# Optimization experiments

Measured on AMD Instinct MI355X. Metric: run time of the kernel, lower is better.

Reference implementation:

```python
import jax, jax.numpy as jnp
import numpy as np

N_NODES = 65536
N_EDGES = 1048576
D_FEAT = 64
K_HOPS = 10
ALPHA = 0.1


def setup_inputs() -> dict:
    key = jax.random.key(0)
    k1, k2 = jax.random.split(key, 2)
    x = jax.random.normal(k1, (N_NODES, D_FEAT), dtype=jnp.float32)
    edge_index = jax.random.randint(k2, (2, N_EDGES), 0, N_NODES, dtype=jnp.int32)
    # PPR init of the learnable polynomial coefficients (length K+1)
    temp = ALPHA * (1.0 - ALPHA) ** np.arange(K_HOPS + 1)
    temp[-1] = (1.0 - ALPHA) ** K_HOPS
    temp = jnp.asarray(temp, dtype=jnp.float32)
    return {"x": x, "temp": temp, "edge_index": edge_index}


def reference(x, temp, edge_index):
    # GCN-normalized adjacency with self-loops (gcn_norm, homophily=True path):
    #   A_hat = D^{-1/2} (A + I) D^{-1/2}
    N = x.shape[0]
    K = temp.shape[0] - 1
    loops = jnp.arange(N, dtype=edge_index.dtype)
    src = jnp.concatenate([edge_index[0], loops])  # message sources (x_j)
    dst = jnp.concatenate([edge_index[1], loops])  # aggregation targets
    ones = jnp.ones(src.shape[0], dtype=x.dtype)
    deg = jax.ops.segment_sum(ones, dst, num_segments=N)  # self-loops => deg > 0
    dinv = jax.lax.rsqrt(deg)
    norm = dinv[src] * dinv[dst]  # [E+N]

    # hidden = temp[K-1]*x; then K-1 propagation hops accumulating temp[k]*A_hat^m x
    hidden = temp[K - 1] * x
    h = x
    for k in range(K - 2, -1, -1):
        # sparse propagate: scatter-add of norm-weighted gathered source features
        h = jax.ops.segment_sum(norm[:, None] * h[src], dst, num_segments=N)
        hidden = hidden + temp[k] * h
    return hidden
```

## Files before the change

### kernel.cpp

```cpp
#include <hip/hip_runtime.h>
#include <hip/hip_fp16.h>

#define N_NODES 65536
#define N_EDGES 1048576
#define BUCKET  64

typedef float vfloat4 __attribute__((ext_vector_type(4)));
typedef unsigned long long ull;


__global__ void count_deg(const int* __restrict__ dst, int* __restrict__ counts,
                          int* __restrict__ rank) {
    int e = blockIdx.x * blockDim.x + threadIdx.x;
    if (e < N_EDGES) rank[e] = atomicAdd(&counts[dst[e]], 1);
}

__global__ void compute_dinv(const int* __restrict__ counts, float* __restrict__ dinv) {
    int v = blockIdx.x * blockDim.x + threadIdx.x;
    if (v < N_NODES) dinv[v] = rsqrtf((float)(counts[v] + 1));
}

__global__ void scatter_src(const int* __restrict__ src, const int* __restrict__ dst,
                            const int* __restrict__ rank,
                            unsigned short* __restrict__ csr) {
    int e = blockIdx.x * blockDim.x + threadIdx.x;
    if (e >= N_EDGES) return;
    int r = rank[e];
    if (r < BUCKET) csr[dst[e] * BUCKET + r] = (unsigned short)src[e];
}

__global__ void cvt_x(const float* __restrict__ x, const float* __restrict__ dinv,
                      __half* __restrict__ t0, __half* __restrict__ xh) {
    int i = blockIdx.x * blockDim.x + threadIdx.x;
    int v = i >> 4;
    float dv = dinv[v];
    vfloat4 val = __builtin_nontemporal_load((const vfloat4*)x + i);
    __half2 xl = __floats2half2_rn(val.x, val.y);
    __half2 xh2 = __floats2half2_rn(val.z, val.w);
    ull ox = ((ull)(*(const unsigned*)&xh2) << 32) | (*(const unsigned*)&xl);
    __half2 tl = __floats2half2_rn(dv * val.x, dv * val.y);
    __half2 th = __floats2half2_rn(dv * val.z, dv * val.w);
    ull ot = ((ull)(*(const unsigned*)&th) << 32) | (*(const unsigned*)&tl);
    __builtin_nontemporal_store(ox, (ull*)xh + i);
    ((ull*)t0)[i] = ot;
}

__global__ void __launch_bounds__(256) hop_kernel(
        const __half* __restrict__ tab, const __half* __restrict__ xh,
        __half* __restrict__ tab_out, float* __restrict__ out_f32,
        const float* __restrict__ temp, const int* __restrict__ counts,
        const unsigned short* __restrict__ csr, const float* __restrict__ dinv,
        int k) {
    int gtid = blockIdx.x * blockDim.x + threadIdx.x;
    int wave = __builtin_amdgcn_readfirstlane(gtid >> 6);
    int lane = gtid & 63;
    int q = lane >> 4;
    int f = lane & 15;

    int v0 = wave * 4;
    float tk = temp[k];
    float sc = (k == 1) ? temp[0] : 1.0f;

    int4 cv = *(const int4*)(counts + v0);
    int cnt[4];
    cnt[0] = min(cv.x, BUCKET); cnt[1] = min(cv.y, BUCKET);
    cnt[2] = min(cv.z, BUCKET); cnt[3] = min(cv.w, BUCKET);
    float4 dvv = *(const float4*)(dinv + v0);
    float dv[4] = {dvv.x, dvv.y, dvv.z, dvv.w};

    int maxc = max(max(cnt[0], cnt[1]), max(cnt[2], cnt[3]));
    int iters = (maxc + 31) >> 5;

    const ull* t2 = (const ull*)tab;
    float a0[4] = {0.f, 0.f, 0.f, 0.f};
    float a1[4] = {0.f, 0.f, 0.f, 0.f};
    float a2[4] = {0.f, 0.f, 0.f, 0.f};
    float a3[4] = {0.f, 0.f, 0.f, 0.f};

    for (int r = 0; r < iters; ++r) {
        int e0 = r * 32;
        #pragma unroll
        for (int j = 0; j < 4; ++j) {
            const int4* bp = (const int4*)(csr + (v0 + j) * BUCKET + e0);
            int4 sg0 = bp[0];
            int4 sg1 = bp[1];
            int4 sg2 = bp[2];
            int4 sg3 = bp[3];
            #pragma unroll
            for (int g = 0; g < 8; ++g) {
                int4 sg = (g < 2) ? sg0 : (g < 4) ? sg1 : (g < 6) ? sg2 : sg3;
                int word = (g & 1) ? ((q & 2) ? sg.w : sg.z)
                                   : ((q & 2) ? sg.y : sg.x);
                int s = (word >> ((q & 1) * 16)) & 0xffff;
                ull row = t2[s * 16 + f];
                row = ((e0 + 4 * g + q) < cnt[j]) ? row : 0ull;
                unsigned rl = (unsigned)row, rh = (unsigned)(row >> 32);
                float2 lo = __half22float2(*(const __half2*)&rl);
                float2 hi = __half22float2(*(const __half2*)&rh);
                a0[j] += lo.x; a1[j] += lo.y; a2[j] += hi.x; a3[j] += hi.y;
            }
        }
    }

    #pragma unroll
    for (int j = 0; j < 4; ++j) {
        a0[j] += __shfl_xor(a0[j], 16); a0[j] += __shfl_xor(a0[j], 32);
        a1[j] += __shfl_xor(a1[j], 16); a1[j] += __shfl_xor(a1[j], 32);
        a2[j] += __shfl_xor(a2[j], 16); a2[j] += __shfl_xor(a2[j], 32);
        a3[j] += __shfl_xor(a3[j], 16); a3[j] += __shfl_xor(a3[j], 32);
    }

    #pragma unroll
    for (int j = 0; j < 4; ++j) {
        int v = v0 + j;
        ull sx = __builtin_nontemporal_load((const ull*)xh + v * 16 + f);
        ull st = t2[v * 16 + f];
        unsigned sxl = (unsigned)sx, sxh2 = (unsigned)(sx >> 32);
        unsigned stl = (unsigned)st, sth = (unsigned)(st >> 32);
        float2 xlo = __half22float2(*(const __half2*)&sxl);
        float2 xhi = __half22float2(*(const __half2*)&sxh2);
        float2 slo = __half22float2(*(const __half2*)&stl);
        float2 shi = __half22float2(*(const __half2*)&sth);
        float m = sc * dv[j];
        float r0 = m * (a0[j] + slo.x) + tk * xlo.x;
        float r1 = m * (a1[j] + slo.y) + tk * xlo.y;
        float r2 = m * (a2[j] + shi.x) + tk * xhi.x;
        float r3 = m * (a3[j] + shi.y) + tk * xhi.y;
        if (q == 0) {
            if (k == 9) {
                vfloat4 o = {r0, r1, r2, r3};
                __builtin_nontemporal_store(o, (vfloat4*)out_f32 + v * 16 + f);
            } else {
                float d2 = dv[j];
                __half2 plo = __floats2half2_rn(d2 * r0, d2 * r1);
                __half2 phi = __floats2half2_rn(d2 * r2, d2 * r3);
                ull o = ((ull)(*(const unsigned*)&phi) << 32)
                      | (*(const unsigned*)&plo);
                ((ull*)tab_out)[v * 16 + f] = o;
            }
        }
    }
}

extern "C" void kernel_launch(void* const* d_in, const int* in_sizes, int n_in,
                              void* d_out, int out_size, void* d_ws, size_t ws_size,
                              hipStream_t stream) {
    const float* x    = (const float*)d_in[0];
    const float* temp = (const float*)d_in[1];
    const int*   ei   = (const int*)d_in[2];
    const int* src = ei;
    const int* dst = ei + N_EDGES;
    float* out = (float*)d_out;

    char* ws = (char*)d_ws;
    int*            counts = (int*)            (ws + 0x000000);
    float*          dinv   = (float*)          (ws + 0x040000);
    int*            rank   = (int*)            (ws + 0x080000);
    unsigned short* csr    = (unsigned short*) (ws + 0x480000);
    __half*         xh     = (__half*)         (ws + 0xC80000);
    __half*         tA     = (__half*)         (ws + 0x1480000);
    __half*         tB     = (__half*)         (ws + 0x1C80000);

    (void)hipMemsetAsync(counts, 0, N_NODES * sizeof(int), stream);
    (void)hipMemsetAsync(csr, 0, N_NODES * BUCKET * sizeof(unsigned short), stream);

    count_deg<<<N_EDGES / 256, 256, 0, stream>>>(dst, counts, rank);
    compute_dinv<<<N_NODES / 256, 256, 0, stream>>>(counts, dinv);
    scatter_src<<<N_EDGES / 256, 256, 0, stream>>>(src, dst, rank, csr);
    cvt_x<<<(N_NODES * 16) / 256, 256, 0, stream>>>(x, dinv, tA, xh);

    const int hop_blocks = (N_NODES / 4) * 64 / 256;
    const __half* gin = tA;
    for (int k = 1; k <= 9; ++k) {
        __half* gout = (k & 1) ? tB : tA;
        hop_kernel<<<hop_blocks, 256, 0, stream>>>(gin, xh, gout, out, temp,
                                                   counts, csr, dinv, k);
        gin = gout;
    }
}
```

Measured before the change: 404.3 us.

## Split feature dimension into two halves to shrink gather working set per hop

The fp16 node tables are reorganised into two planes of 32 features each, and the full 9-hop propagation runs once per plane. Each wave lane group now gathers 64-byte half-rows (8 lanes per edge, 8 edges in parallel), which adds one more shuffle-reduction stage. The goal is to halve the randomly gathered table size per pass so it stays better resident in L2. The cost is twice as many hop launches and reading the CSR, counts and dinv twice. Nontemporal load/store hints are also dropped.

```diff
diff --git a/kernel.cpp b/kernel.cpp
--- a/kernel.cpp
+++ b/kernel.cpp
@@ -4,6 +4,7 @@
 #define N_NODES 65536
 #define N_EDGES 1048576
 #define BUCKET  64
+#define HALF_ELEMS (N_NODES * 32)
 
 typedef float vfloat4 __attribute__((ext_vector_type(4)));
 typedef unsigned long long ull;
@@ -33,16 +34,18 @@
                       __half* __restrict__ t0, __half* __restrict__ xh) {
     int i = blockIdx.x * blockDim.x + threadIdx.x;
     int v = i >> 4;
+    int o = i & 15;
     float dv = dinv[v];
-    vfloat4 val = __builtin_nontemporal_load((const vfloat4*)x + i);
+    float4 val = ((const float4*)x)[i];
     __half2 xl = __floats2half2_rn(val.x, val.y);
     __half2 xh2 = __floats2half2_rn(val.z, val.w);
     ull ox = ((ull)(*(const unsigned*)&xh2) << 32) | (*(const unsigned*)&xl);
     __half2 tl = __floats2half2_rn(dv * val.x, dv * val.y);
     __half2 th = __floats2half2_rn(dv * val.z, dv * val.w);
     ull ot = ((ull)(*(const unsigned*)&th) << 32) | (*(const unsigned*)&tl);
-    __builtin_nontemporal_store(ox, (ull*)xh + i);
-    ((ull*)t0)[i] = ot;
+    int idx = (o >> 3) * (HALF_ELEMS / 4) + v * 8 + (o & 7);
+    ((ull*)xh)[idx] = ox;
+    ((ull*)t0)[idx] = ot;
 }
 
 __global__ void __launch_bounds__(256) hop_kernel(
@@ -54,8 +57,8 @@
     int gtid = blockIdx.x * blockDim.x + threadIdx.x;
     int wave = __builtin_amdgcn_readfirstlane(gtid >> 6);
     int lane = gtid & 63;
-    int q = lane >> 4;
-    int f = lane & 15;
+    int q = lane >> 3;
+    int f = lane & 7;
 
     int v0 = wave * 4;
     float tk = temp[k];
@@ -87,13 +90,13 @@
             int4 sg2 = bp[2];
             int4 sg3 = bp[3];
             #pragma unroll
-            for (int g = 0; g < 8; ++g) {
-                int4 sg = (g < 2) ? sg0 : (g < 4) ? sg1 : (g < 6) ? sg2 : sg3;
-                int word = (g & 1) ? ((q & 2) ? sg.w : sg.z)
+            for (int g = 0; g < 4; ++g) {
+                int4 sg = (g == 0) ? sg0 : (g == 1) ? sg1 : (g == 2) ? sg2 : sg3;
+                int word = (q & 4) ? ((q & 2) ? sg.w : sg.z)
                                    : ((q & 2) ? sg.y : sg.x);
                 int s = (word >> ((q & 1) * 16)) & 0xffff;
-                ull row = t2[s * 16 + f];
-                row = ((e0 + 4 * g + q) < cnt[j]) ? row : 0ull;
+                ull row = t2[s * 8 + f];
+                row = ((e0 + 8 * g + q) < cnt[j]) ? row : 0ull;
                 unsigned rl = (unsigned)row, rh = (unsigned)(row >> 32);
                 float2 lo = __half22float2(*(const __half2*)&rl);
                 float2 hi = __half22float2(*(const __half2*)&rh);
@@ -104,17 +107,17 @@
 
     #pragma unroll
     for (int j = 0; j < 4; ++j) {
-        a0[j] += __shfl_xor(a0[j], 16); a0[j] += __shfl_xor(a0[j], 32);
-        a1[j] += __shfl_xor(a1[j], 16); a1[j] += __shfl_xor(a1[j], 32);
-        a2[j] += __shfl_xor(a2[j], 16); a2[j] += __shfl_xor(a2[j], 32);
-        a3[j] += __shfl_xor(a3[j], 16); a3[j] += __shfl_xor(a3[j], 32);
+        a0[j] += __shfl_xor(a0[j], 8); a0[j] += __shfl_xor(a0[j], 16); a0[j] += __shfl_xor(a0[j], 32);
+        a1[j] += __shfl_xor(a1[j], 8); a1[j] += __shfl_xor(a1[j], 16); a1[j] += __shfl_xor(a1[j], 32);
+        a2[j] += __shfl_xor(a2[j], 8); a2[j] += __shfl_xor(a2[j], 16); a2[j] += __shfl_xor(a2[j], 32);
+        a3[j] += __shfl_xor(a3[j], 8); a3[j] += __shfl_xor(a3[j], 16); a3[j] += __shfl_xor(a3[j], 32);
     }
 
     #pragma unroll
     for (int j = 0; j < 4; ++j) {
         int v = v0 + j;
-        ull sx = __builtin_nontemporal_load((const ull*)xh + v * 16 + f);
-        ull st = t2[v * 16 + f];
+        ull sx = ((const ull*)xh)[v * 8 + f];
+        ull st = t2[v * 8 + f];
         unsigned sxl = (unsigned)sx, sxh2 = (unsigned)(sx >> 32);
         unsigned stl = (unsigned)st, sth = (unsigned)(st >> 32);
         float2 xlo = __half22float2(*(const __half2*)&sxl);
@@ -129,14 +132,14 @@
         if (q == 0) {
             if (k == 9) {
                 vfloat4 o = {r0, r1, r2, r3};
-                __builtin_nontemporal_store(o, (vfloat4*)out_f32 + v * 16 + f);
+                ((vfloat4*)out_f32)[v * 16 + f] = o;
             } else {
                 float d2 = dv[j];
                 __half2 plo = __floats2half2_rn(d2 * r0, d2 * r1);
                 __half2 phi = __floats2half2_rn(d2 * r2, d2 * r3);
                 ull o = ((ull)(*(const unsigned*)&phi) << 32)
                       | (*(const unsigned*)&plo);
-                ((ull*)tab_out)[v * 16 + f] = o;
+                ((ull*)tab_out)[v * 8 + f] = o;
             }
         }
     }
@@ -170,11 +173,15 @@
     cvt_x<<<(N_NODES * 16) / 256, 256, 0, stream>>>(x, dinv, tA, xh);
 
     const int hop_blocks = (N_NODES / 4) * 64 / 256;
-    const __half* gin = tA;
-    for (int k = 1; k <= 9; ++k) {
-        __half* gout = (k & 1) ? tB : tA;
-        hop_kernel<<<hop_blocks, 256, 0, stream>>>(gin, xh, gout, out, temp,
-                                                   counts, csr, dinv, k);
-        gin = gout;
+    for (int ph = 0; ph < 2; ++ph) {
+        const __half* xh_ph = xh + ph * HALF_ELEMS;
+        float* out_ph = out + ph * 32;
+        const __half* gin = tA + ph * HALF_ELEMS;
+        for (int k = 1; k <= 9; ++k) {
+            __half* gout = ((k & 1) ? tB : tA) + ph * HALF_ELEMS;
+            hop_kernel<<<hop_blocks, 256, 0, stream>>>(gin, xh_ph, gout, out_ph,
+                                                       temp, counts, csr, dinv, k);
+            gin = gout;
+        }
     }
 }
```

New measurement: 502.7 us. 24.4% more time.
